# Performance work log

Hardware: AMD Instinct MI355X
Metric: run time of the kernel (lower is better)

## Reference

```python
import jax, jax.numpy as jnp
import numpy as np

N, E, F_IN, F_OUT = 16384, 4096, 128, 128
EPS = 1e-6


def setup_inputs() -> dict:
    key = jax.random.key(0)
    k1, k2, k3 = jax.random.split(key, 3)
    H = (jax.random.uniform(k1, (N, E)) < 0.05).astype(jnp.float32)
    x = jax.random.normal(k2, (N, F_IN), dtype=jnp.float32)
    W = jax.random.normal(k3, (F_IN, F_OUT), dtype=jnp.float32) * 0.05
    return {"x": x, "H": H, "W": W}


def reference(x, H, W):
    # D_v^{-1} H D_e^{-1} H^T x W, computed without materializing the NxN
    # adjacency: diagonal matmuls become row/col broadcast scaling, and the
    # GEMM chain is reordered right-to-left (same math, associativity).
    d_e_inv = 1.0 / (H.sum(axis=0) + EPS)   # [E]
    d_v_inv = 1.0 / (H.sum(axis=1) + EPS)   # [N]
    xw = x @ W                               # [N, F_out]
    edge_msg = H.T @ xw                      # [E, F_out] gather onto edges
    edge_msg = d_e_inv[:, None] * edge_msg   # D_e^{-1}
    node_msg = H @ edge_msg                  # [N, F_out] scatter back to nodes
    return d_v_inv[:, None] * node_msg       # D_v^{-1}
```

## Files before the change

### kernel.cpp

```cpp
#include <hip/hip_runtime.h>
#include <stdint.h>

#define N_NODES 16384
#define N_EDGES 4096
#define FDIM    128
#define EPSF    1e-6f

typedef __attribute__((ext_vector_type(8))) short short8;
typedef __attribute__((ext_vector_type(4))) float f32x4;
typedef unsigned long long ull;

__device__ __forceinline__ unsigned short f2bf(float f) {
    uint32_t u = __float_as_uint(f);
    return (unsigned short)((u + 0x7FFFu + ((u >> 16) & 1u)) >> 16);
}

__device__ __forceinline__ short8 as_s8(uint4 v) {
    union { uint4 a; short8 b; } u; u.a = v; return u.b;
}

__device__ __forceinline__ short8 expand8(uint32_t half, int bitoff) {
    uint32_t b8 = (half >> bitoff) & 0xFFu;
    uint32_t lo = ((b8 & 0xFu) * 0x00204081u) & 0x01010101u;
    uint32_t hi = ((b8 >> 4) * 0x00204081u) & 0x01010101u;
    union { short8 v; uint32_t u[4]; } a;
#if __has_builtin(__builtin_amdgcn_perm)
    a.u[0] = __builtin_amdgcn_perm(0u, lo, 0x04010400u) * 0x3F80u;
    a.u[1] = __builtin_amdgcn_perm(0u, lo, 0x04030402u) * 0x3F80u;
    a.u[2] = __builtin_amdgcn_perm(0u, hi, 0x04010400u) * 0x3F80u;
    a.u[3] = __builtin_amdgcn_perm(0u, hi, 0x04030402u) * 0x3F80u;
#else
    a.u[0] = ((lo & 1u)         | ((lo >> 8) & 1u) << 16) * 0x3F80u;
    a.u[1] = (((lo >> 16) & 1u) | ((lo >> 24) & 1u) << 16) * 0x3F80u;
    a.u[2] = ((hi & 1u)         | ((hi >> 8) & 1u) << 16) * 0x3F80u;
    a.u[3] = (((hi >> 16) & 1u) | ((hi >> 24) & 1u) << 16) * 0x3F80u;
#endif
    return a.v;
}

__global__ __launch_bounds__(256) void k_bitpack(const float* __restrict__ H,
        ull* __restrict__ bitsNE, float* __restrict__ dvinv) {
    int w = threadIdx.x >> 6, lane = threadIdx.x & 63;
    int n = blockIdx.x * 4 + w;
    const float4* hr = (const float4*)(H + (size_t)n * N_EDGES);
    ull* out = bitsNE + (size_t)n * (N_EDGES / 64);
    int cnt = 0;
    for (int c4 = 0; c4 < N_EDGES / 256; ++c4) {
        float4 v = hr[c4 * 64 + lane];
        ull b0 = __ballot(v.x > 0.5f);
        ull b1 = __ballot(v.y > 0.5f);
        ull b2 = __ballot(v.z > 0.5f);
        ull b3 = __ballot(v.w > 0.5f);
        cnt += __popcll(b0) + __popcll(b1) + __popcll(b2) + __popcll(b3);
        if (lane == 0) {
            #pragma unroll
            for (int q = 0; q < 4; ++q) {
                ull wq = ((b0 >> (16 * q)) & 0xFFFFull)
                       | (((b1 >> (16 * q)) & 0xFFFFull) << 16)
                       | (((b2 >> (16 * q)) & 0xFFFFull) << 32)
                       | (((b3 >> (16 * q)) & 0xFFFFull) << 48);
                out[c4 * 4 + q] = wq;
            }
        }
    }
    if (lane == 0) dvinv[n] = 1.0f / ((float)cnt + EPSF);
}

__global__ __launch_bounds__(256) void k_transpose(const ull* __restrict__ bitsNE,
        ull* __restrict__ bitsEN) {
    int w = threadIdx.x >> 6, lane = threadIdx.x & 63;
    int wid = blockIdx.x * 4 + w;
    int et = wid & 63, nt = wid >> 6;
    int pl = 4 * (lane & 15) + (lane >> 4);
    ull q = bitsNE[(size_t)(nt * 64 + pl) * (N_EDGES / 64) + et];
    ull outv = 0;
    for (int j = 0; j < 64; ++j) {
        ull r = __ballot((int)((q >> j) & 1ULL));
        if (lane == j) outv = r;
    }
    bitsEN[(size_t)(et * 64 + pl) * (N_NODES / 64) + nt] = outv;
}

__global__ __launch_bounds__(256) void k_edeg(const ull* __restrict__ bitsEN,
        float* __restrict__ deinv) {
    int w = threadIdx.x >> 6, lane = threadIdx.x & 63;
    int e = blockIdx.x * 4 + w;
    const ull* r = bitsEN + (size_t)e * (N_NODES / 64);
    int s = __popcll(r[lane]) + __popcll(r[lane + 64]) + __popcll(r[lane + 128]) + __popcll(r[lane + 192]);
    for (int o = 32; o; o >>= 1) s += __shfl_xor(s, o);
    if (lane == 0) deinv[e] = 1.0f / ((float)s + EPSF);
}

__global__ __launch_bounds__(256) void k_xw(const float* __restrict__ x, const float* __restrict__ W,
        unsigned short* __restrict__ xwTp) {
    __shared__ __attribute__((aligned(16))) unsigned short ldsWT[128 * 136];
    __shared__ __attribute__((aligned(16))) unsigned short ldsT[128 * 72];
    int t = threadIdx.x, lane = t & 63, w = t >> 6;
    int r16 = lane & 15, klane = lane >> 4;
    for (int i = 0; i < 64; ++i) {
        int idx = i * 256 + t;
        int k = idx >> 7, f = idx & 127;
        ldsWT[f * 136 + k] = f2bf(W[idx]);
    }
    __syncthreads();
    int nbase = blockIdx.x * 64;
    int row = nbase + w * 16 + r16;
    const float4* xr4 = (const float4*)(x + (size_t)row * FDIM);
    f32x4 acc[8] = {};
    for (int kb = 0; kb < 128; kb += 32) {
        float4 u0 = xr4[(kb >> 2) + klane * 2];
        float4 u1 = xr4[(kb >> 2) + klane * 2 + 1];
        union { short8 v; unsigned short u[8]; } a;
        a.u[0] = f2bf(u0.x); a.u[1] = f2bf(u0.y); a.u[2] = f2bf(u0.z); a.u[3] = f2bf(u0.w);
        a.u[4] = f2bf(u1.x); a.u[5] = f2bf(u1.y); a.u[6] = f2bf(u1.z); a.u[7] = f2bf(u1.w);
        #pragma unroll
        for (int fb = 0; fb < 8; ++fb) {
            short8 b = *(const short8*)&ldsWT[(fb * 16 + r16) * 136 + kb + klane * 8];
            acc[fb] = __builtin_amdgcn_mfma_f32_16x16x32_bf16(a.v, b, acc[fb], 0, 0, 0);
        }
    }
    #pragma unroll
    for (int fb = 0; fb < 8; ++fb)
        #pragma unroll
        for (int r = 0; r < 4; ++r)
            ldsT[(fb * 16 + r16) * 72 + 16 * r + w * 4 + klane] = f2bf(acc[fb][r]);
    __syncthreads();
    int f = t >> 1, part = t & 1;
    #pragma unroll
    for (int j = 0; j < 4; ++j)
        *(uint4*)&xwTp[(size_t)f * N_NODES + nbase + part * 32 + j * 8] =
            *(const uint4*)&ldsT[f * 72 + part * 32 + j * 8];
}

#define LOADP(Q0, Q1, BUF, p) do { \
    Q0 = brow0[(p)]; Q1 = brow1[(p)]; \
    const unsigned short* _src = bcol + (size_t)(p) * 64; \
    _Pragma("unroll") \
    for (int _fb = 0; _fb < 4; ++_fb) { \
        BUF[_fb * 2]     = *(const uint4*)(_src + _fb * fbstride); \
        BUF[_fb * 2 + 1] = *(const uint4*)(_src + _fb * fbstride + 32); \
    } } while (0)

#define COMPUTEP(Q0, Q1, BUF) do { \
    _Pragma("unroll") \
    for (int _s = 0; _s < 2; ++_s) { \
        uint32_t _h0 = (uint32_t)(_s == 0 ? (Q0) : ((Q0) >> 32)); \
        uint32_t _h1 = (uint32_t)(_s == 0 ? (Q1) : ((Q1) >> 32)); \
        short8 _a0 = expand8(_h0, bitoff); \
        short8 _a1 = expand8(_h1, bitoff); \
        _Pragma("unroll") \
        for (int _fb = 0; _fb < 4; ++_fb) { \
            short8 _b = as_s8(BUF[_fb * 2 + _s]); \
            acc[0][_fb] = __builtin_amdgcn_mfma_f32_16x16x32_bf16(_a0, _b, acc[0][_fb], 0, 0, 0); \
            acc[1][_fb] = __builtin_amdgcn_mfma_f32_16x16x32_bf16(_a1, _b, acc[1][_fb], 0, 0, 0); \
        } } } while (0)

template<bool FINAL>
__global__ __launch_bounds__(256) void k_gemm_bits(
        const ull* __restrict__ bits, int krows,
        const unsigned short* __restrict__ BT, int K,
        float* __restrict__ Cout, const float* __restrict__ rowScale,
        int M, int pairs) {
    int t = threadIdx.x, lane = t & 63, w = t >> 6;
    int r16 = lane & 15, klane = lane >> 4;
    int bitoff = klane * 8;
    int wm = w >> 1, wf = w & 1;
    int mbase = blockIdx.x * 64 + wm * 32;
    int kw0 = blockIdx.z * pairs;
    const ull* brow0 = bits + (size_t)(mbase + r16) * krows + kw0;
    const ull* brow1 = brow0 + (size_t)16 * krows;
    const unsigned short* bcol = BT + (size_t)(wf * 64 + r16) * K + (size_t)kw0 * 64 + klane * 8;
    const int fbstride = 16 * K;

    f32x4 acc[2][4] = {};
    ull qA0, qA1, qB0, qB1;
    uint4 bufA[8], bufB[8];

    LOADP(qA0, qA1, bufA, 0);
    for (int p = 0; p < pairs; p += 2) {
        LOADP(qB0, qB1, bufB, p + 1);
        COMPUTEP(qA0, qA1, bufA);
        if (p + 2 < pairs) LOADP(qA0, qA1, bufA, p + 2);
        COMPUTEP(qB0, qB1, bufB);
    }

    #pragma unroll
    for (int fr = 0; fr < 2; ++fr)
        #pragma unroll
        for (int fb = 0; fb < 4; ++fb)
            #pragma unroll
            for (int r = 0; r < 4; ++r) {
                int row = mbase + fr * 16 + klane * 4 + r;
                int col = wf * 64 + fb * 16 + r16;
                float v = acc[fr][fb][r];
                if (FINAL)
                    Cout[(size_t)row * FDIM + col] = rowScale[row] * v;
                else
                    Cout[(size_t)blockIdx.z * M * FDIM + (size_t)row * FDIM + col] = v;
            }
}

__global__ __launch_bounds__(256) void k_reduce_scale_T(const float* __restrict__ partials,
        const float* __restrict__ deinv, unsigned short* __restrict__ emTp, int S) {
    __shared__ float lds[64 * 129];
    int t = threadIdx.x;
    int e0 = blockIdx.x * 64;
    for (int i = 0; i < 32; ++i) {
        int idx = i * 256 + t;
        int e_l = idx >> 7, f = idx & 127;
        float s = 0.f;
        for (int z = 0; z < S; ++z)
            s += partials[(size_t)z * N_EDGES * FDIM + (size_t)(e0 + e_l) * FDIM + f];
        lds[e_l * 129 + f] = s * deinv[e0 + e_l];
    }
    __syncthreads();
    for (int i = 0; i < 32; ++i) {
        int idx = i * 256 + t;
        int f = idx >> 6, j = idx & 63;
        int pj = 4 * (j & 15) + (j >> 4);
        emTp[(size_t)f * N_EDGES + e0 + j] = f2bf(lds[pj * 129 + f]);
    }
}

extern "C" void kernel_launch(void* const* d_in, const int* in_sizes, int n_in,
                              void* d_out, int out_size, void* d_ws, size_t ws_size,
                              hipStream_t stream) {
    const float* x = (const float*)d_in[0];
    const float* H = (const float*)d_in[1];
    const float* W = (const float*)d_in[2];
    float* out = (float*)d_out;
    char* ws = (char*)d_ws;

    ull* bitsNE = (ull*)(ws);
    ull* bitsEN = (ull*)(ws + (8u << 20));
    unsigned short* xwTp = (unsigned short*)(ws + (16u << 20));
    unsigned short* emTp = (unsigned short*)(ws + (20u << 20));
    float* dvinv = (float*)(ws + (21u << 20));
    float* deinv = (float*)(ws + (21u << 20) + 65536);
    size_t pbase = (21u << 20) + 65536 + 16384;
    float* partials = (float*)(ws + pbase);

    int S = 4;
    while (S > 1 && pbase + (size_t)S * N_EDGES * FDIM * 4 > ws_size) S >>= 1;

    hipLaunchKernelGGL(k_bitpack, dim3(4096), dim3(256), 0, stream, H, bitsNE, dvinv);
    hipLaunchKernelGGL(k_transpose, dim3(4096), dim3(256), 0, stream, bitsNE, bitsEN);
    hipLaunchKernelGGL(k_edeg, dim3(1024), dim3(256), 0, stream, bitsEN, deinv);
    hipLaunchKernelGGL(k_xw, dim3(256), dim3(256), 0, stream, x, W, xwTp);
    hipLaunchKernelGGL((k_gemm_bits<false>), dim3(64, 1, S), dim3(256), 0, stream,
                       bitsEN, N_NODES / 64, xwTp, N_NODES, partials, (const float*)nullptr,
                       N_EDGES, (N_NODES / 64) / S);
    hipLaunchKernelGGL(k_reduce_scale_T, dim3(64), dim3(256), 0, stream, partials, deinv, emTp, S);
    hipLaunchKernelGGL((k_gemm_bits<true>), dim3(256, 1, 1), dim3(256), 0, stream,
                       bitsNE, N_EDGES / 64, emTp, N_EDGES, out, dvinv,
                       N_NODES, N_EDGES / 64);
}
```

Baseline: 264.6 us.

## Use butterfly bit-transpose and deeper split-K for both bit GEMMs

Replaces the 64-step ballot loop in the bit-matrix transpose with a six-step shuffle butterfly, and has each wave process eight tiles. The first GEMM's split-K factor goes from 4 to 8. The second GEMM gets a 2-way split-K with a new reduce-and-scale kernel when workspace allows. Launch bounds now request 2 blocks per CU. The aim is more parallelism on a GPU that these grids underfill (64 and 256 blocks), at the cost of extra partial-sum traffic and one more launch.

```diff
diff --git a/kernel.cpp b/kernel.cpp
--- a/kernel.cpp
+++ b/kernel.cpp
@@ -14,7 +14,6 @@
     uint32_t u = __float_as_uint(f);
     return (unsigned short)((u + 0x7FFFu + ((u >> 16) & 1u)) >> 16);
 }
-
 __device__ __forceinline__ short8 as_s8(uint4 v) {
     union { uint4 a; short8 b; } u; u.a = v; return u.b;
 }
@@ -36,6 +35,18 @@
     a.u[3] = (((hi >> 16) & 1u) | ((hi >> 24) & 1u) << 16) * 0x3F80u;
 #endif
     return a.v;
+}
+
+__device__ __forceinline__ ull bit_transpose64(ull q, int lane) {
+    const ull M32 = 0xFFFFFFFF00000000ull, M16 = 0xFFFF0000FFFF0000ull,
+              M8 = 0xFF00FF00FF00FF00ull, M4 = 0xF0F0F0F0F0F0F0F0ull,
+              M2 = 0xCCCCCCCCCCCCCCCCull, M1 = 0xAAAAAAAAAAAAAAAAull;
+#define TSTEP(d, Md) { ull tv = __shfl_xor(q, d, 64); \
+    q = ((lane & d) == 0) ? ((q & ~Md) | ((tv << d) & Md)) \
+                          : ((q & Md) | ((tv >> d) & ~Md)); }
+    TSTEP(32, M32) TSTEP(16, M16) TSTEP(8, M8) TSTEP(4, M4) TSTEP(2, M2) TSTEP(1, M1)
+#undef TSTEP
+    return q;
 }
 
 __global__ __launch_bounds__(256) void k_bitpack(const float* __restrict__ H,
@@ -66,19 +77,20 @@
     if (lane == 0) dvinv[n] = 1.0f / ((float)cnt + EPSF);
 }
 
-__global__ __launch_bounds__(256) void k_transpose(const ull* __restrict__ bitsNE,
+__global__ __launch_bounds__(256) void k_transpose_bf(const ull* __restrict__ bitsNE,
         ull* __restrict__ bitsEN) {
     int w = threadIdx.x >> 6, lane = threadIdx.x & 63;
     int wid = blockIdx.x * 4 + w;
-    int et = wid & 63, nt = wid >> 6;
+    int nt = wid >> 3, etg = wid & 7;
     int pl = 4 * (lane & 15) + (lane >> 4);
-    ull q = bitsNE[(size_t)(nt * 64 + pl) * (N_EDGES / 64) + et];
-    ull outv = 0;
-    for (int j = 0; j < 64; ++j) {
-        ull r = __ballot((int)((q >> j) & 1ULL));
-        if (lane == j) outv = r;
-    }
-    bitsEN[(size_t)(et * 64 + pl) * (N_NODES / 64) + nt] = outv;
+    const ull* src = bitsNE + (size_t)(nt * 64 + pl) * (N_EDGES / 64);
+    #pragma unroll
+    for (int i = 0; i < 8; ++i) {
+        int et = etg * 8 + i;
+        ull q = src[et];
+        q = bit_transpose64(q, lane);
+        bitsEN[(size_t)(et * 64 + pl) * (N_NODES / 64) + nt] = q;
+    }
 }
 
 __global__ __launch_bounds__(256) void k_edeg(const ull* __restrict__ bitsEN,
@@ -143,47 +155,44 @@
 
 #define COMPUTEP(Q0, Q1, BUF) do { \
     _Pragma("unroll") \
-    for (int _s = 0; _s < 2; ++_s) { \
-        uint32_t _h0 = (uint32_t)(_s == 0 ? (Q0) : ((Q0) >> 32)); \
-        uint32_t _h1 = (uint32_t)(_s == 0 ? (Q1) : ((Q1) >> 32)); \
+    for (int _s2 = 0; _s2 < 2; ++_s2) { \
+        uint32_t _h0 = (uint32_t)(_s2 == 0 ? (Q0) : ((Q0) >> 32)); \
+        uint32_t _h1 = (uint32_t)(_s2 == 0 ? (Q1) : ((Q1) >> 32)); \
         short8 _a0 = expand8(_h0, bitoff); \
         short8 _a1 = expand8(_h1, bitoff); \
         _Pragma("unroll") \
-        for (int _fb = 0; _fb < 4; ++_fb) { \
-            short8 _b = as_s8(BUF[_fb * 2 + _s]); \
-            acc[0][_fb] = __builtin_amdgcn_mfma_f32_16x16x32_bf16(_a0, _b, acc[0][_fb], 0, 0, 0); \
-            acc[1][_fb] = __builtin_amdgcn_mfma_f32_16x16x32_bf16(_a1, _b, acc[1][_fb], 0, 0, 0); \
+        for (int _f = 0; _f < 4; ++_f) { \
+            short8 _b = as_s8(BUF[_f * 2 + _s2]); \
+            acc[0][_f] = __builtin_amdgcn_mfma_f32_16x16x32_bf16(_a0, _b, acc[0][_f], 0, 0, 0); \
+            acc[1][_f] = __builtin_amdgcn_mfma_f32_16x16x32_bf16(_a1, _b, acc[1][_f], 0, 0, 0); \
         } } } while (0)
 
 template<bool FINAL>
-__global__ __launch_bounds__(256) void k_gemm_bits(
+__global__ __launch_bounds__(256, 2) void k_gemm_gen(
         const ull* __restrict__ bits, int krows,
         const unsigned short* __restrict__ BT, int K,
         float* __restrict__ Cout, const float* __restrict__ rowScale,
-        int M, int pairs) {
+        int M, int npairs) {
     int t = threadIdx.x, lane = t & 63, w = t >> 6;
     int r16 = lane & 15, klane = lane >> 4;
     int bitoff = klane * 8;
     int wm = w >> 1, wf = w & 1;
     int mbase = blockIdx.x * 64 + wm * 32;
-    int kw0 = blockIdx.z * pairs;
-    const ull* brow0 = bits + (size_t)(mbase + r16) * krows + kw0;
+    int kq0 = blockIdx.z * npairs;
+    const ull* brow0 = bits + (size_t)(mbase + r16) * krows + kq0;
     const ull* brow1 = brow0 + (size_t)16 * krows;
-    const unsigned short* bcol = BT + (size_t)(wf * 64 + r16) * K + (size_t)kw0 * 64 + klane * 8;
-    const int fbstride = 16 * K;
-
+    const unsigned short* bcol = BT + (size_t)(wf * 64 + r16) * K + (size_t)kq0 * 64 + klane * 8;
+    const size_t fbstride = (size_t)16 * K;
     f32x4 acc[2][4] = {};
     ull qA0, qA1, qB0, qB1;
     uint4 bufA[8], bufB[8];
-
     LOADP(qA0, qA1, bufA, 0);
-    for (int p = 0; p < pairs; p += 2) {
+    for (int p = 0; p < npairs; p += 2) {
         LOADP(qB0, qB1, bufB, p + 1);
         COMPUTEP(qA0, qA1, bufA);
-        if (p + 2 < pairs) LOADP(qA0, qA1, bufA, p + 2);
+        if (p + 2 < npairs) LOADP(qA0, qA1, bufA, p + 2);
         COMPUTEP(qB0, qB1, bufB);
     }
-
     #pragma unroll
     for (int fr = 0; fr < 2; ++fr)
         #pragma unroll
@@ -222,6 +231,22 @@
     }
 }
 
+__global__ __launch_bounds__(256) void k_finalN(const float* __restrict__ partN,
+        const float* __restrict__ dvinv, float* __restrict__ out) {
+    const float4* pa = (const float4*)partN;
+    const float4* pb = (const float4*)(partN + (size_t)N_NODES * FDIM);
+    float4* o4 = (float4*)out;
+    int t = threadIdx.x;
+    #pragma unroll
+    for (int i = 0; i < 4; ++i) {
+        int idx = blockIdx.x * 1024 + i * 256 + t;
+        float4 a = pa[idx], b = pb[idx];
+        float s = dvinv[idx >> 5];
+        o4[idx] = make_float4((a.x + b.x) * s, (a.y + b.y) * s,
+                              (a.z + b.z) * s, (a.w + b.w) * s);
+    }
+}
+
 extern "C" void kernel_launch(void* const* d_in, const int* in_sizes, int n_in,
                               void* d_out, int out_size, void* d_ws, size_t ws_size,
                               hipStream_t stream) {
@@ -237,21 +262,29 @@
     unsigned short* emTp = (unsigned short*)(ws + (20u << 20));
     float* dvinv = (float*)(ws + (21u << 20));
     float* deinv = (float*)(ws + (21u << 20) + 65536);
-    size_t pbase = (21u << 20) + 65536 + 16384;
-    float* partials = (float*)(ws + pbase);
-
-    int S = 4;
-    while (S > 1 && pbase + (size_t)S * N_EDGES * FDIM * 4 > ws_size) S >>= 1;
+    float* partE = (float*)(ws + (22u << 20));
+    float* partN = (float*)(ws + (38u << 20));
+
+    int SE = 8;
+    while (SE > 1 && (22u << 20) + (size_t)SE * N_EDGES * FDIM * 4 > ws_size) SE >>= 1;
+    bool sn2 = ws_size >= ((38u << 20) + (size_t)2 * N_NODES * FDIM * 4);
 
     hipLaunchKernelGGL(k_bitpack, dim3(4096), dim3(256), 0, stream, H, bitsNE, dvinv);
-    hipLaunchKernelGGL(k_transpose, dim3(4096), dim3(256), 0, stream, bitsNE, bitsEN);
+    hipLaunchKernelGGL(k_transpose_bf, dim3(512), dim3(256), 0, stream, bitsNE, bitsEN);
     hipLaunchKernelGGL(k_edeg, dim3(1024), dim3(256), 0, stream, bitsEN, deinv);
     hipLaunchKernelGGL(k_xw, dim3(256), dim3(256), 0, stream, x, W, xwTp);
-    hipLaunchKernelGGL((k_gemm_bits<false>), dim3(64, 1, S), dim3(256), 0, stream,
-                       bitsEN, N_NODES / 64, xwTp, N_NODES, partials, (const float*)nullptr,
-                       N_EDGES, (N_NODES / 64) / S);
-    hipLaunchKernelGGL(k_reduce_scale_T, dim3(64), dim3(256), 0, stream, partials, deinv, emTp, S);
-    hipLaunchKernelGGL((k_gemm_bits<true>), dim3(256, 1, 1), dim3(256), 0, stream,
-                       bitsNE, N_EDGES / 64, emTp, N_EDGES, out, dvinv,
-                       N_NODES, N_EDGES / 64);
-}
+    hipLaunchKernelGGL((k_gemm_gen<false>), dim3(64, 1, SE), dim3(256), 0, stream,
+                       bitsEN, N_NODES / 64, xwTp, N_NODES, partE, (const float*)nullptr,
+                       N_EDGES, (N_NODES / 64) / SE);
+    hipLaunchKernelGGL(k_reduce_scale_T, dim3(64), dim3(256), 0, stream, partE, deinv, emTp, SE);
+    if (sn2) {
+        hipLaunchKernelGGL((k_gemm_gen<false>), dim3(256, 1, 2), dim3(256), 0, stream,
+                           bitsNE, N_EDGES / 64, emTp, N_EDGES, partN, (const float*)nullptr,
+                           N_NODES, (N_EDGES / 64) / 2);
+        hipLaunchKernelGGL(k_finalN, dim3(512), dim3(256), 0, stream, partN, dvinv, out);
+    } else {
+        hipLaunchKernelGGL((k_gemm_gen<true>), dim3(256, 1, 1), dim3(256), 0, stream,
+                           bitsNE, N_EDGES / 64, emTp, N_EDGES, out, dvinv,
+                           N_NODES, N_EDGES / 64);
+    }
+}
```

New measurement: 302.2 us. 1.14x slower.
